# Kernel tuning notes

Measured on AMD Instinct MI355X. Metric: run time of the kernel, lower is better.

The kernel has to match this reference:

```python
import jax, jax.numpy as jnp
import numpy as np

B, S, D, H = 8, 1024, 512, 8
DK = D // H
NEG = -1e30  # stands in for -inf; masked probs are zero-filled afterwards, so math matches


def setup_inputs() -> dict:
    rng = jax.random.key(0)
    ks = jax.random.split(rng, 12)
    f = lambda k, shape: jax.random.normal(k, shape, dtype=jnp.float32)
    w = lambda k: f(k, (D, D)) * 0.02  # stored as (in, out); y = x @ W + b
    return {
        "query": f(ks[0], (B, S, D)),
        "key": f(ks[1], (B, S, D)),
        "value": f(ks[2], (B, S, D)),
        "mask": jax.random.randint(ks[3], (B, 1, S), 0, 2, dtype=jnp.int32),
        "Wq": w(ks[4]), "bq": jnp.zeros((D,), jnp.float32),
        "Wk": w(ks[5]), "bk": jnp.zeros((D,), jnp.float32),
        "Wv": w(ks[6]), "bv": jnp.zeros((D,), jnp.float32),
        "Wo": w(ks[7]), "bo": jnp.zeros((D,), jnp.float32),
    }


def reference(query, key, value, mask, Wq, bq, Wk, bk, Wv, bv, Wo, bo):
    # QKV projections -> (B, H, S, DK)
    def proj(x, W, b):
        return (x @ W + b).reshape(B, -1, H, DK).transpose(0, 2, 1, 3)

    q = proj(query, Wq, bq)
    k = proj(key, Wk, bk)
    v = proj(value, Wv, bv)

    scores = jnp.einsum("bhqd,bhkd->bhqk", q, k) / jnp.sqrt(jnp.float32(DK))
    m = (mask[:, None, :, :] == 0)  # (B, 1, 1, S): True where masked out
    scores = jnp.where(m, NEG, scores)
    attn = jax.nn.softmax(scores, axis=-1)
    attn = jnp.where(m, 0.0, attn)  # dropout rate is 0.0 -> identity

    x = jnp.einsum("bhqk,bhkd->bhqd", attn, v)
    x = x.transpose(0, 2, 1, 3).reshape(B, -1, D)  # (B, S, D)
    return x @ Wo + bo
```

## Files before the change

### kernel.cpp

```cpp
#include <hip/hip_runtime.h>
#include <hip/hip_bf16.h>

#define NB 8
#define NS 1024
#define ND 512
#define NH 8
#define NDK 64

typedef __attribute__((ext_vector_type(8))) short bf16x8;
typedef __attribute__((ext_vector_type(4))) float f32x4;
typedef __attribute__((ext_vector_type(16))) float f32x16;

#define QSCALE 0.18033688011112042f
#define NEGBIG -3.0e38f

#define CVTPK(dst, a, b) \
    asm("v_cvt_pk_bf16_f32 %0, %1, %2" : "=v"(dst) : "v"(a), "v"(b))
#define PLSWAP(a, b) \
    asm("v_permlane32_swap_b32 %0, %1" : "+v"(a), "+v"(b))

__device__ __forceinline__ unsigned short bfround(float f) {
    union { float f; unsigned u; } v; v.f = f;
    unsigned u = v.u;
    u += 0x7fffu + ((u >> 16) & 1u);
    return (unsigned short)(u >> 16);
}


__global__ __launch_bounds__(256) void wt_kernel(const float* __restrict__ W0,
                                                 const float* __restrict__ W1,
                                                 const float* __restrict__ W2,
                                                 const float* __restrict__ W3,
                                                 unsigned short* __restrict__ wt) {
    __shared__ float sh[64][65];
    const int z = blockIdx.z;
    const float* W = z == 0 ? W0 : z == 1 ? W1 : z == 2 ? W2 : W3;
    unsigned short* out = wt + (size_t)z * ND * ND;
    const int o0 = blockIdx.x * 64, i0 = blockIdx.y * 64;
    const int tx = threadIdx.x & 63;
    const int ty = threadIdx.x >> 6;
    #pragma unroll
    for (int rr = 0; rr < 16; ++rr) {
        const int row = ty * 16 + rr;
        sh[row][tx] = W[(size_t)(i0 + row) * ND + o0 + tx];
    }
    __syncthreads();
    #pragma unroll
    for (int rr = 0; rr < 16; ++rr) {
        const int row = ty * 16 + rr;
        out[(size_t)(o0 + row) * ND + i0 + tx] = bfround(sh[tx][row]);
    }
}

__global__ __launch_bounds__(256) void gemm_qkv(
    const float* __restrict__ A0, const float* __restrict__ A1, const float* __restrict__ A2,
    const unsigned short* __restrict__ wt,
    const float* __restrict__ b0, const float* __restrict__ b1, const float* __restrict__ b2,
    unsigned short* __restrict__ outb) {
    __shared__ unsigned short SM[27648];
    const int t = threadIdx.x;
    const int lane = t & 63, w = t >> 6;
    const int wr = w >> 1, wc = w & 1;
    const int lr = lane & 15, lg = lane >> 4;
    const int bid = blockIdx.x;
    const int u = (bid & 7) * 32 + (bid >> 3);
    const int xt = u & 3, yt = u >> 2;
    const int z = blockIdx.y;
    const float* A = z == 0 ? A0 : z == 1 ? A1 : A2;
    const float* bias = z == 0 ? b0 : z == 1 ? b1 : b2;
    const unsigned short* Wt = wt + (size_t)z * ND * ND;
    unsigned short* outp = outb + (size_t)z * NB * NH * NS * NDK;
    const int m0 = yt * 128, n0 = xt * 128;

    const int a_row = t >> 4;
    const int a_col = (t & 15) * 4;
    const int b_row = t >> 3;
    const int b_col = (t & 7) * 8;

    f32x4 acc[4][4];
    #pragma unroll
    for (int i = 0; i < 4; ++i)
        #pragma unroll
        for (int j = 0; j < 4; ++j) acc[i][j] = (f32x4){0.f, 0.f, 0.f, 0.f};

    f32x4 ra[8];
    bf16x8 rbv[4];

#define AL(p) (SM + (p) * 9216)
#define BLS (SM + 18432)

#define QKV_LOAD(kt) do {                                                      \
        const int _k0 = (kt) * 64;                                             \
        _Pragma("unroll")                                                      \
        for (int j = 0; j < 8; ++j)                                            \
            ra[j] = *(const f32x4*)(A + (size_t)(m0 + a_row + j * 16) * ND + _k0 + a_col); \
        _Pragma("unroll")                                                      \
        for (int j = 0; j < 4; ++j)                                            \
            rbv[j] = *(const bf16x8*)(Wt + (size_t)(n0 + b_row + j * 32) * ND + _k0 + b_col); \
    } while (0)

#define QKV_WRITEA(p) do {                                                     \
        _Pragma("unroll")                                                      \
        for (int j = 0; j < 8; ++j) {                                          \
            unsigned c0, c1;                                                   \
            CVTPK(c0, ra[j][0], ra[j][1]);                                     \
            CVTPK(c1, ra[j][2], ra[j][3]);                                     \
            uint2 pv; pv.x = c0; pv.y = c1;                                    \
            *(uint2*)(&AL(p)[(a_row + j * 16) * 72 + a_col]) = pv;             \
        }                                                                      \
    } while (0)

#define QKV_WRITEB() do {                                                      \
        _Pragma("unroll")                                                      \
        for (int j = 0; j < 4; ++j)                                            \
            *(bf16x8*)(&BLS[(b_row + j * 32) * 72 + b_col]) = rbv[j];          \
    } while (0)

#define QKV_COMPUTE(p) do {                                                    \
        _Pragma("unroll")                                                      \
        for (int kk = 0; kk < 2; ++kk) {                                       \
            bf16x8 af[4], bfr[4];                                              \
            _Pragma("unroll")                                                  \
            for (int mi = 0; mi < 4; ++mi)                                     \
                af[mi] = *(const bf16x8*)(&AL(p)[(wr * 64 + mi * 16 + lr) * 72 + kk * 32 + lg * 8]); \
            _Pragma("unroll")                                                  \
            for (int nj = 0; nj < 4; ++nj)                                     \
                bfr[nj] = *(const bf16x8*)(&BLS[(wc * 64 + nj * 16 + lr) * 72 + kk * 32 + lg * 8]); \
            __builtin_amdgcn_s_setprio(1);                                     \
            _Pragma("unroll")                                                  \
            for (int mi = 0; mi < 4; ++mi)                                     \
                _Pragma("unroll")                                              \
                for (int nj = 0; nj < 4; ++nj)                                 \
                    acc[mi][nj] = __builtin_amdgcn_mfma_f32_16x16x32_bf16(     \
                        af[mi], bfr[nj], acc[mi][nj], 0, 0, 0);                \
            __builtin_amdgcn_s_setprio(0);                                     \
        }                                                                      \
    } while (0)

    QKV_LOAD(0);
    QKV_WRITEA(0);
    QKV_WRITEB();
    QKV_LOAD(1);
    __builtin_amdgcn_sched_barrier(0);
    __syncthreads();
    #pragma unroll 1
    for (int kt = 0; kt < 7; ++kt) {
        QKV_COMPUTE(kt & 1);
        __syncthreads();
        QKV_WRITEA((kt + 1) & 1);
        QKV_WRITEB();
        QKV_LOAD(kt + 2 > 7 ? 7 : kt + 2);
        __builtin_amdgcn_sched_barrier(0);
        __syncthreads();
    }
    QKV_COMPUTE(1);
#undef QKV_LOAD
#undef QKV_WRITEA
#undef QKV_WRITEB
#undef QKV_COMPUTE
#undef AL
#undef BLS

    __syncthreads();
    const float osc = z == 0 ? QSCALE : 1.0f;
    const int bb = m0 >> 10;
    const unsigned msb = (unsigned)(m0 & 1023);
    char* const C = (char*)SM;
    if (z <= 1) {
        #pragma unroll
        for (int mi = 0; mi < 4; ++mi)
            #pragma unroll
            for (int nj = 0; nj < 4; ++nj) {
                const int coln = wc * 64 + nj * 16 + lr;
                const float bv = bias[n0 + coln];
                #pragma unroll
                for (int r = 0; r < 4; ++r) {
                    const int row = wr * 64 + mi * 16 + lg * 4 + r;
                    unsigned off = (unsigned)(row * 256 + coln * 2);
                    off ^= (row & 7) << 4;
                    *(unsigned short*)(C + off) = bfround((acc[mi][nj][r] + bv) * osc);
                }
            }
        __syncthreads();
        #pragma unroll
        for (int cc = 0; cc < 8; ++cc) {
            const int c = w * 8 + cc;
            const int sg = c >> 3, hhl = (c >> 2) & 1, kk = c & 3;
            const int row = sg * 32 + (lane & 31);
            unsigned off = (unsigned)(row * 256 + (hhl * 64 + kk * 16 + (lane >> 5) * 8) * 2);
            off ^= (row & 7) << 4;
            const bf16x8 v8 = *(const bf16x8*)(C + off);
            const int hh = xt * 2 + hhl;
            const unsigned chunk = z == 0 ? ((msb >> 5) + sg) * 4 + kk
                                          : ((msb >> 6) + (sg >> 1)) * 8 + (sg & 1) * 4 + kk;
            *(bf16x8*)(outp + (((size_t)(bb * NH + hh)) << 16) +
                       (size_t)chunk * 512 + lane * 8) = v8;
        }
    } else {
        #pragma unroll
        for (int mi = 0; mi < 4; ++mi)
            #pragma unroll
            for (int nj = 0; nj < 4; ++nj) {
                const int dkl = wc * 64 + nj * 16 + lr;
                const float bv = bias[n0 + dkl];
                #pragma unroll
                for (int r = 0; r < 4; ++r) {
                    const int sl = wr * 64 + mi * 16 + lg * 4 + r;
                    unsigned off = (unsigned)(dkl * 256 + sl * 2);
                    off ^= (dkl & 7) << 4;
                    *(unsigned short*)(C + off) = bfround(acc[mi][nj][r] + bv);
                }
            }
        __syncthreads();
        #pragma unroll
        for (int cc = 0; cc < 8; ++cc) {
            const int c = w * 8 + cc;
            const int hhl = c >> 4, s6 = (c >> 3) & 1, od = (c >> 2) & 1, s4 = c & 3;
            const int row = hhl * 64 + od * 32 + (lane & 31);
            unsigned off = (unsigned)(row * 256 + (s6 * 64 + s4 * 16 + (lane >> 5) * 8) * 2);
            off ^= (row & 7) << 4;
            const bf16x8 v8 = *(const bf16x8*)(C + off);
            const int hh = xt * 2 + hhl;
            const unsigned chunk = ((msb >> 6) + s6) * 8 + od * 4 + s4;
            *(bf16x8*)(outp + (((size_t)(bb * NH + hh)) << 16) +
                       (size_t)chunk * 512 + lane * 8) = v8;
        }
    }
}

__global__ __launch_bounds__(256) void gemm_out(
    const unsigned short* __restrict__ Xb, const unsigned short* __restrict__ Wt,
    const float* __restrict__ bo, float* __restrict__ outp) {
    __shared__ unsigned short SM2[10240];
    const int t = threadIdx.x;
    const int lane = t & 63, w = t >> 6;
    const int wr = w >> 1, wc = w & 1;
    const int lr = lane & 15, lg = lane >> 4;
    const int bid = blockIdx.x;
    const int u = (bid & 7) * 128 + (bid >> 3);
    const int xt = u & 7, yt = u >> 3;
    const int m0 = yt * 64, n0 = xt * 64;

    const int s_row = t >> 2;
    const int s_col = (t & 3) * 8;

    f32x4 acc[2][2];
    #pragma unroll
    for (int i = 0; i < 2; ++i)
        #pragma unroll
        for (int j = 0; j < 2; ++j) acc[i][j] = (f32x4){0.f, 0.f, 0.f, 0.f};

    bf16x8 raa, rbb;

#define OUT_LOAD(kt) do {                                                      \
        const int _k0 = (kt) * 32;                                             \
        raa = *(const bf16x8*)(Xb + (size_t)(m0 + s_row) * ND + _k0 + s_col);  \
        rbb = *(const bf16x8*)(Wt + (size_t)(n0 + s_row) * ND + _k0 + s_col);  \
    } while (0)

#define OUT_WRITE(p) do {                                                      \
        *(bf16x8*)(&SM2[(p) * 2560 + s_row * 40 + s_col]) = raa;               \
        *(bf16x8*)(&SM2[5120 + (p) * 2560 + s_row * 40 + s_col]) = rbb;        \
    } while (0)

#define OUT_COMPUTE(p) do {                                                    \
        bf16x8 af[2], bfr[2];                                                  \
        _Pragma("unroll")                                                      \
        for (int mi = 0; mi < 2; ++mi)                                         \
            af[mi] = *(const bf16x8*)(&SM2[(p) * 2560 + (wr * 32 + mi * 16 + lr) * 40 + lg * 8]); \
        _Pragma("unroll")                                                      \
        for (int nj = 0; nj < 2; ++nj)                                         \
            bfr[nj] = *(const bf16x8*)(&SM2[5120 + (p) * 2560 + (wc * 32 + nj * 16 + lr) * 40 + lg * 8]); \
        __builtin_amdgcn_s_setprio(1);                                         \
        _Pragma("unroll")                                                      \
        for (int mi = 0; mi < 2; ++mi)                                         \
            _Pragma("unroll")                                                  \
            for (int nj = 0; nj < 2; ++nj)                                     \
                acc[mi][nj] = __builtin_amdgcn_mfma_f32_16x16x32_bf16(         \
                    af[mi], bfr[nj], acc[mi][nj], 0, 0, 0);                    \
        __builtin_amdgcn_s_setprio(0);                                         \
    } while (0)

    OUT_LOAD(0);
    OUT_WRITE(0);
    OUT_LOAD(1);
    __syncthreads();
    #pragma unroll 1
    for (int kt = 0; kt < 15; ++kt) {
        OUT_COMPUTE(kt & 1);
        OUT_WRITE((kt + 1) & 1);
        if (kt < 14) OUT_LOAD(kt + 2);
        __syncthreads();
    }
    OUT_COMPUTE(1);
#undef OUT_LOAD
#undef OUT_WRITE
#undef OUT_COMPUTE

    #pragma unroll
    for (int mi = 0; mi < 2; ++mi) {
        #pragma unroll
        for (int nj = 0; nj < 2; ++nj) {
            const int n = n0 + wc * 32 + nj * 16 + lr;
            const float bv = bo[n];
            #pragma unroll
            for (int r = 0; r < 4; ++r) {
                const int m = m0 + wr * 32 + mi * 16 + lg * 4 + r;
                outp[(size_t)m * ND + n] = acc[mi][nj][r] + bv;
            }
        }
    }
}

struct AttnState {
    f32x16 acc0, acc1;
    float m_st, l_st;
};

__device__ __forceinline__ void attn_step(const bf16x8 (&kf)[8], const bf16x8 (&vv)[8],
                                          const bf16x8 (&qf)[4], int mval,
                                          float* __restrict__ brow, int lane, int hi,
                                          AttnState& st) {
    brow[lane] = mval ? 0.f : NEGBIG;

    f32x16 sc0 = {}, sc1 = {};
    __builtin_amdgcn_s_setprio(1);
    sc0 = __builtin_amdgcn_mfma_f32_32x32x16_bf16(kf[0], qf[0], sc0, 0, 0, 0);
    sc1 = __builtin_amdgcn_mfma_f32_32x32x16_bf16(kf[4], qf[0], sc1, 0, 0, 0);
    sc0 = __builtin_amdgcn_mfma_f32_32x32x16_bf16(kf[1], qf[1], sc0, 0, 0, 0);
    sc1 = __builtin_amdgcn_mfma_f32_32x32x16_bf16(kf[5], qf[1], sc1, 0, 0, 0);
    sc0 = __builtin_amdgcn_mfma_f32_32x32x16_bf16(kf[2], qf[2], sc0, 0, 0, 0);
    sc1 = __builtin_amdgcn_mfma_f32_32x32x16_bf16(kf[6], qf[2], sc1, 0, 0, 0);
    sc0 = __builtin_amdgcn_mfma_f32_32x32x16_bf16(kf[3], qf[3], sc0, 0, 0, 0);
    sc1 = __builtin_amdgcn_mfma_f32_32x32x16_bf16(kf[7], qf[3], sc1, 0, 0, 0);
    __builtin_amdgcn_s_setprio(0);

    {
        const float* bl = brow + 4 * hi;
        #pragma unroll
        for (int mm = 0; mm < 4; ++mm) {
            const f32x4 bv0 = *(const f32x4*)(bl + 8 * mm);
            const f32x4 bv1 = *(const f32x4*)(bl + 32 + 8 * mm);
            #pragma unroll
            for (int c = 0; c < 4; ++c) {
                sc0[4 * mm + c] += bv0[c];
                sc1[4 * mm + c] += bv1[c];
            }
        }
    }

    float tv[16];
    #pragma unroll
    for (int r = 0; r < 16; ++r) tv[r] = fmaxf(sc0[r], sc1[r]);
    #pragma unroll
    for (int s = 8; s > 0; s >>= 1)
        #pragma unroll
        for (int r = 0; r < 16; ++r)
            if (r < s) tv[r] = fmaxf(tv[r], tv[r + s]);
    const float mx = fmaxf(tv[0], __shfl_xor(tv[0], 32));
    const float mn = fmaxf(st.m_st, mx);

    #pragma unroll
    for (int r = 0; r < 16; ++r) {
        sc0[r] = __builtin_amdgcn_exp2f(sc0[r] - mn);
        sc1[r] = __builtin_amdgcn_exp2f(sc1[r] - mn);
    }
    #pragma unroll
    for (int r = 0; r < 16; ++r) tv[r] = sc0[r] + sc1[r];
    #pragma unroll
    for (int s = 8; s > 0; s >>= 1)
        #pragma unroll
        for (int r = 0; r < 16; ++r)
            if (r < s) tv[r] += tv[r + s];
    const float rs = tv[0] + __shfl_xor(tv[0], 32);

    const bool ch = mn > st.m_st;
    if (__any(ch)) {
        const float f = __builtin_amdgcn_exp2f(st.m_st - mn);
        st.l_st = st.l_st * f + rs;
        st.m_st = mn;
        #pragma unroll
        for (int r = 0; r < 16; ++r) { st.acc0[r] *= f; st.acc1[r] *= f; }
    } else {
        st.l_st += rs;
    }

    union U8 { unsigned u[4]; bf16x8 v; };
    bf16x8 pA0, pA1, pB0, pB1;
    {
        unsigned w00, w01, w10, w11, w20, w21, w30, w31;
        CVTPK(w00, sc0[0], sc0[1]);  CVTPK(w01, sc0[2], sc0[3]);
        CVTPK(w10, sc0[4], sc0[5]);  CVTPK(w11, sc0[6], sc0[7]);
        CVTPK(w20, sc0[8], sc0[9]);  CVTPK(w21, sc0[10], sc0[11]);
        CVTPK(w30, sc0[12], sc0[13]); CVTPK(w31, sc0[14], sc0[15]);
        PLSWAP(w00, w10); PLSWAP(w01, w11);
        PLSWAP(w20, w30); PLSWAP(w21, w31);
        U8 f0; f0.u[0] = w00; f0.u[1] = w01; f0.u[2] = w10; f0.u[3] = w11;
        U8 f1; f1.u[0] = w20; f1.u[1] = w21; f1.u[2] = w30; f1.u[3] = w31;
        pA0 = f0.v; pA1 = f1.v;
    }
    {
        unsigned w00, w01, w10, w11, w20, w21, w30, w31;
        CVTPK(w00, sc1[0], sc1[1]);  CVTPK(w01, sc1[2], sc1[3]);
        CVTPK(w10, sc1[4], sc1[5]);  CVTPK(w11, sc1[6], sc1[7]);
        CVTPK(w20, sc1[8], sc1[9]);  CVTPK(w21, sc1[10], sc1[11]);
        CVTPK(w30, sc1[12], sc1[13]); CVTPK(w31, sc1[14], sc1[15]);
        PLSWAP(w00, w10); PLSWAP(w01, w11);
        PLSWAP(w20, w30); PLSWAP(w21, w31);
        U8 f0; f0.u[0] = w00; f0.u[1] = w01; f0.u[2] = w10; f0.u[3] = w11;
        U8 f1; f1.u[0] = w20; f1.u[1] = w21; f1.u[2] = w30; f1.u[3] = w31;
        pB0 = f0.v; pB1 = f1.v;
    }

    __builtin_amdgcn_s_setprio(1);
    st.acc0 = __builtin_amdgcn_mfma_f32_32x32x16_bf16(vv[0], pA0, st.acc0, 0, 0, 0);
    st.acc1 = __builtin_amdgcn_mfma_f32_32x32x16_bf16(vv[4], pA0, st.acc1, 0, 0, 0);
    st.acc0 = __builtin_amdgcn_mfma_f32_32x32x16_bf16(vv[1], pA1, st.acc0, 0, 0, 0);
    st.acc1 = __builtin_amdgcn_mfma_f32_32x32x16_bf16(vv[5], pA1, st.acc1, 0, 0, 0);
    st.acc0 = __builtin_amdgcn_mfma_f32_32x32x16_bf16(vv[2], pB0, st.acc0, 0, 0, 0);
    st.acc1 = __builtin_amdgcn_mfma_f32_32x32x16_bf16(vv[6], pB0, st.acc1, 0, 0, 0);
    st.acc0 = __builtin_amdgcn_mfma_f32_32x32x16_bf16(vv[3], pB1, st.acc0, 0, 0, 0);
    st.acc1 = __builtin_amdgcn_mfma_f32_32x32x16_bf16(vv[7], pB1, st.acc1, 0, 0, 0);
    __builtin_amdgcn_s_setprio(0);
}

__global__ __launch_bounds__(256, 2) void attn_kernel(const unsigned short* __restrict__ QF,
                                                      const unsigned short* __restrict__ KF,
                                                      const unsigned short* __restrict__ VF,
                                                      const int* __restrict__ mask,
                                                      unsigned short* __restrict__ Xb) {
    __shared__ float bias_lds[4][64];
    const int t = threadIdx.x;
    const int lane = t & 63, w = t >> 6;
    const int q32 = lane & 31, hi = lane >> 5;
    const int bid = blockIdx.x;
    const int u = (bid & 7) * 64 + (bid >> 3);
    const int bh = u >> 3, xq = u & 7;
    const int b = bh >> 3, h = bh & 7;
    const int q = xq * 128 + w * 32 + q32;
    const unsigned short* QFh = QF + ((size_t)bh << 16);
    const unsigned short* KFh = KF + ((size_t)bh << 16);
    const unsigned short* VFh = VF + ((size_t)bh << 16);
    const int* mk = mask + b * NS;
    float* brow = &bias_lds[w][0];

    bf16x8 qf[4];
    {
        const unsigned short* Qp = QFh + (size_t)(xq * 16 + w * 4) * 512 + lane * 8;
        qf[0] = *(const bf16x8*)(Qp + 0 * 512);
        qf[1] = *(const bf16x8*)(Qp + 1 * 512);
        qf[2] = *(const bf16x8*)(Qp + 2 * 512);
        qf[3] = *(const bf16x8*)(Qp + 3 * 512);
    }

    AttnState st;
    st.acc0 = (f32x16){}; st.acc1 = (f32x16){};
    st.m_st = -1.0e30f; st.l_st = 0.f;

    bf16x8 kA[8], kB[8], vv[8];

#define LOADK(dst, itx) do {                                                   \
        const unsigned short* _p = KFh + (size_t)(itx) * 4096 + lane * 8;      \
        dst[0] = *(const bf16x8*)(_p + 0 * 512);                               \
        dst[1] = *(const bf16x8*)(_p + 1 * 512);                               \
        dst[2] = *(const bf16x8*)(_p + 2 * 512);                               \
        dst[3] = *(const bf16x8*)(_p + 3 * 512);                               \
        dst[4] = *(const bf16x8*)(_p + 4 * 512);                               \
        dst[5] = *(const bf16x8*)(_p + 5 * 512);                               \
        dst[6] = *(const bf16x8*)(_p + 6 * 512);                               \
        dst[7] = *(const bf16x8*)(_p + 7 * 512);                               \
    } while (0)

#define LOADV(dst, itx) do {                                                   \
        const unsigned short* _p = VFh + (size_t)(itx) * 4096 + lane * 8;      \
        dst[0] = *(const bf16x8*)(_p + 0 * 512);                               \
        dst[1] = *(const bf16x8*)(_p + 1 * 512);                               \
        dst[2] = *(const bf16x8*)(_p + 2 * 512);                               \
        dst[3] = *(const bf16x8*)(_p + 3 * 512);                               \
        dst[4] = *(const bf16x8*)(_p + 4 * 512);                               \
        dst[5] = *(const bf16x8*)(_p + 5 * 512);                               \
        dst[6] = *(const bf16x8*)(_p + 6 * 512);                               \
        dst[7] = *(const bf16x8*)(_p + 7 * 512);                               \
    } while (0)

    LOADK(kA, 0);
    #pragma unroll 1
    for (int ii = 0; ii < 8; ++ii) {
        const int itE = ii * 2, itO = itE + 1;
        const int mE = mk[itE * 64 + lane];
        LOADV(vv, itE);
        LOADK(kB, itO);
        __builtin_amdgcn_sched_barrier(0);
        attn_step(kA, vv, qf, mE, brow, lane, hi, st);
        const int mO = mk[itO * 64 + lane];
        const int itN = itO + 1 > 15 ? 15 : itO + 1;
        LOADV(vv, itO);
        LOADK(kA, itN);
        __builtin_amdgcn_sched_barrier(0);
        attn_step(kB, vv, qf, mO, brow, lane, hi, st);
    }
#undef LOADK
#undef LOADV

    const float inv = st.l_st > 0.f ? 1.f / st.l_st : 0.f;
    unsigned short* Xp = Xb + (size_t)(b * NS + q) * ND + h * 64 + 4 * hi;
    #pragma unroll
    for (int mm = 0; mm < 4; ++mm) {
        unsigned w0, w1;
        CVTPK(w0, st.acc0[4 * mm] * inv, st.acc0[4 * mm + 1] * inv);
        CVTPK(w1, st.acc0[4 * mm + 2] * inv, st.acc0[4 * mm + 3] * inv);
        uint2 pv; pv.x = w0; pv.y = w1;
        *(uint2*)(Xp + 8 * mm) = pv;
        CVTPK(w0, st.acc1[4 * mm] * inv, st.acc1[4 * mm + 1] * inv);
        CVTPK(w1, st.acc1[4 * mm + 2] * inv, st.acc1[4 * mm + 3] * inv);
        pv.x = w0; pv.y = w1;
        *(uint2*)(Xp + 32 + 8 * mm) = pv;
    }
}

extern "C" void kernel_launch(void* const* d_in, const int* in_sizes, int n_in,
                              void* d_out, int out_size, void* d_ws, size_t ws_size,
                              hipStream_t stream) {
    const float* query = (const float*)d_in[0];
    const float* key   = (const float*)d_in[1];
    const float* value = (const float*)d_in[2];
    const int*   mask  = (const int*)d_in[3];
    const float* Wq = (const float*)d_in[4];
    const float* bq = (const float*)d_in[5];
    const float* Wk = (const float*)d_in[6];
    const float* bk = (const float*)d_in[7];
    const float* Wv = (const float*)d_in[8];
    const float* bv = (const float*)d_in[9];
    const float* Wo = (const float*)d_in[10];
    const float* bo = (const float*)d_in[11];

    const size_t HEADSZ = (size_t)NB * NH * NS * NDK;
    unsigned short* wt = (unsigned short*)d_ws;
    unsigned short* QFb = wt + (size_t)4 * ND * ND;
    unsigned short* KFb = QFb + HEADSZ;
    unsigned short* VFb = KFb + HEADSZ;
    unsigned short* Xb  = VFb + HEADSZ;

    wt_kernel<<<dim3(8, 8, 4), 256, 0, stream>>>(Wq, Wk, Wv, Wo, wt);

    gemm_qkv<<<dim3(256, 3), 256, 0, stream>>>(query, key, value, wt, bq, bk, bv, QFb);

    attn_kernel<<<512, 256, 0, stream>>>(QFb, KFb, VFb, mask, Xb);

    gemm_out<<<1024, 256, 0, stream>>>(Xb, wt + (size_t)3 * ND * ND, bo, (float*)d_out);
}
```

Measured before the change: 77.76 us.

## Stage K/V tiles through LDS with async global_load_lds double buffering

The attention kernel stops having each wave load the full K and V tiles from global memory into registers. Instead the four waves of a block cooperatively copy each 64-key K/V tile into a double-buffered LDS area with global_load_lds, wait on vmcnt and a barrier, then read the fragments from LDS. This cuts redundant global/L2 traffic across waves sharing a head. The mask bias for all keys is now precomputed once into LDS, and launch bounds rise to allow three blocks per CU. In exchange it adds two block barriers per iteration and more LDS use per block, which may limit overlap and occupancy.

```diff
diff --git a/kernel.cpp b/kernel.cpp
--- a/kernel.cpp
+++ b/kernel.cpp
@@ -18,6 +18,15 @@
     asm("v_cvt_pk_bf16_f32 %0, %1, %2" : "=v"(dst) : "v"(a), "v"(b))
 #define PLSWAP(a, b) \
     asm("v_permlane32_swap_b32 %0, %1" : "+v"(a), "+v"(b))
+#define GLOAD16(gp, lp)                                                        \
+    __builtin_amdgcn_global_load_lds(                                          \
+        (const __attribute__((address_space(1))) unsigned*)(gp),               \
+        (__attribute__((address_space(3))) unsigned*)(lp), 16, 0, 0)
+#define VMCNT0() asm volatile("s_waitcnt vmcnt(0)" ::: "memory")
+#define VMCNT4() asm volatile("s_waitcnt vmcnt(4)" ::: "memory")
+#define LGKM0()  asm volatile("s_waitcnt lgkmcnt(0)" ::: "memory")
+#define SBAR() __builtin_amdgcn_s_barrier()
+#define SCHED0() __builtin_amdgcn_sched_barrier(0)
 
 __device__ __forceinline__ unsigned short bfround(float f) {
     union { float f; unsigned u; } v; v.f = f;
@@ -182,6 +191,8 @@
                 }
             }
         __syncthreads();
+        const unsigned cb = 0;
+        (void)cb;
         #pragma unroll
         for (int cc = 0; cc < 8; ++cc) {
             const int c = w * 8 + cc;
@@ -312,124 +323,13 @@
     }
 }
 
-struct AttnState {
-    f32x16 acc0, acc1;
-    float m_st, l_st;
-};
-
-__device__ __forceinline__ void attn_step(const bf16x8 (&kf)[8], const bf16x8 (&vv)[8],
-                                          const bf16x8 (&qf)[4], int mval,
-                                          float* __restrict__ brow, int lane, int hi,
-                                          AttnState& st) {
-    brow[lane] = mval ? 0.f : NEGBIG;
-
-    f32x16 sc0 = {}, sc1 = {};
-    __builtin_amdgcn_s_setprio(1);
-    sc0 = __builtin_amdgcn_mfma_f32_32x32x16_bf16(kf[0], qf[0], sc0, 0, 0, 0);
-    sc1 = __builtin_amdgcn_mfma_f32_32x32x16_bf16(kf[4], qf[0], sc1, 0, 0, 0);
-    sc0 = __builtin_amdgcn_mfma_f32_32x32x16_bf16(kf[1], qf[1], sc0, 0, 0, 0);
-    sc1 = __builtin_amdgcn_mfma_f32_32x32x16_bf16(kf[5], qf[1], sc1, 0, 0, 0);
-    sc0 = __builtin_amdgcn_mfma_f32_32x32x16_bf16(kf[2], qf[2], sc0, 0, 0, 0);
-    sc1 = __builtin_amdgcn_mfma_f32_32x32x16_bf16(kf[6], qf[2], sc1, 0, 0, 0);
-    sc0 = __builtin_amdgcn_mfma_f32_32x32x16_bf16(kf[3], qf[3], sc0, 0, 0, 0);
-    sc1 = __builtin_amdgcn_mfma_f32_32x32x16_bf16(kf[7], qf[3], sc1, 0, 0, 0);
-    __builtin_amdgcn_s_setprio(0);
-
-    {
-        const float* bl = brow + 4 * hi;
-        #pragma unroll
-        for (int mm = 0; mm < 4; ++mm) {
-            const f32x4 bv0 = *(const f32x4*)(bl + 8 * mm);
-            const f32x4 bv1 = *(const f32x4*)(bl + 32 + 8 * mm);
-            #pragma unroll
-            for (int c = 0; c < 4; ++c) {
-                sc0[4 * mm + c] += bv0[c];
-                sc1[4 * mm + c] += bv1[c];
-            }
-        }
-    }
-
-    float tv[16];
-    #pragma unroll
-    for (int r = 0; r < 16; ++r) tv[r] = fmaxf(sc0[r], sc1[r]);
-    #pragma unroll
-    for (int s = 8; s > 0; s >>= 1)
-        #pragma unroll
-        for (int r = 0; r < 16; ++r)
-            if (r < s) tv[r] = fmaxf(tv[r], tv[r + s]);
-    const float mx = fmaxf(tv[0], __shfl_xor(tv[0], 32));
-    const float mn = fmaxf(st.m_st, mx);
-
-    #pragma unroll
-    for (int r = 0; r < 16; ++r) {
-        sc0[r] = __builtin_amdgcn_exp2f(sc0[r] - mn);
-        sc1[r] = __builtin_amdgcn_exp2f(sc1[r] - mn);
-    }
-    #pragma unroll
-    for (int r = 0; r < 16; ++r) tv[r] = sc0[r] + sc1[r];
-    #pragma unroll
-    for (int s = 8; s > 0; s >>= 1)
-        #pragma unroll
-        for (int r = 0; r < 16; ++r)
-            if (r < s) tv[r] += tv[r + s];
-    const float rs = tv[0] + __shfl_xor(tv[0], 32);
-
-    const bool ch = mn > st.m_st;
-    if (__any(ch)) {
-        const float f = __builtin_amdgcn_exp2f(st.m_st - mn);
-        st.l_st = st.l_st * f + rs;
-        st.m_st = mn;
-        #pragma unroll
-        for (int r = 0; r < 16; ++r) { st.acc0[r] *= f; st.acc1[r] *= f; }
-    } else {
-        st.l_st += rs;
-    }
-
-    union U8 { unsigned u[4]; bf16x8 v; };
-    bf16x8 pA0, pA1, pB0, pB1;
-    {
-        unsigned w00, w01, w10, w11, w20, w21, w30, w31;
-        CVTPK(w00, sc0[0], sc0[1]);  CVTPK(w01, sc0[2], sc0[3]);
-        CVTPK(w10, sc0[4], sc0[5]);  CVTPK(w11, sc0[6], sc0[7]);
-        CVTPK(w20, sc0[8], sc0[9]);  CVTPK(w21, sc0[10], sc0[11]);
-        CVTPK(w30, sc0[12], sc0[13]); CVTPK(w31, sc0[14], sc0[15]);
-        PLSWAP(w00, w10); PLSWAP(w01, w11);
-        PLSWAP(w20, w30); PLSWAP(w21, w31);
-        U8 f0; f0.u[0] = w00; f0.u[1] = w01; f0.u[2] = w10; f0.u[3] = w11;
-        U8 f1; f1.u[0] = w20; f1.u[1] = w21; f1.u[2] = w30; f1.u[3] = w31;
-        pA0 = f0.v; pA1 = f1.v;
-    }
-    {
-        unsigned w00, w01, w10, w11, w20, w21, w30, w31;
-        CVTPK(w00, sc1[0], sc1[1]);  CVTPK(w01, sc1[2], sc1[3]);
-        CVTPK(w10, sc1[4], sc1[5]);  CVTPK(w11, sc1[6], sc1[7]);
-        CVTPK(w20, sc1[8], sc1[9]);  CVTPK(w21, sc1[10], sc1[11]);
-        CVTPK(w30, sc1[12], sc1[13]); CVTPK(w31, sc1[14], sc1[15]);
-        PLSWAP(w00, w10); PLSWAP(w01, w11);
-        PLSWAP(w20, w30); PLSWAP(w21, w31);
-        U8 f0; f0.u[0] = w00; f0.u[1] = w01; f0.u[2] = w10; f0.u[3] = w11;
-        U8 f1; f1.u[0] = w20; f1.u[1] = w21; f1.u[2] = w30; f1.u[3] = w31;
-        pB0 = f0.v; pB1 = f1.v;
-    }
-
-    __builtin_amdgcn_s_setprio(1);
-    st.acc0 = __builtin_amdgcn_mfma_f32_32x32x16_bf16(vv[0], pA0, st.acc0, 0, 0, 0);
-    st.acc1 = __builtin_amdgcn_mfma_f32_32x32x16_bf16(vv[4], pA0, st.acc1, 0, 0, 0);
-    st.acc0 = __builtin_amdgcn_mfma_f32_32x32x16_bf16(vv[1], pA1, st.acc0, 0, 0, 0);
-    st.acc1 = __builtin_amdgcn_mfma_f32_32x32x16_bf16(vv[5], pA1, st.acc1, 0, 0, 0);
-    st.acc0 = __builtin_amdgcn_mfma_f32_32x32x16_bf16(vv[2], pB0, st.acc0, 0, 0, 0);
-    st.acc1 = __builtin_amdgcn_mfma_f32_32x32x16_bf16(vv[6], pB0, st.acc1, 0, 0, 0);
-    st.acc0 = __builtin_amdgcn_mfma_f32_32x32x16_bf16(vv[3], pB1, st.acc0, 0, 0, 0);
-    st.acc1 = __builtin_amdgcn_mfma_f32_32x32x16_bf16(vv[7], pB1, st.acc1, 0, 0, 0);
-    __builtin_amdgcn_s_setprio(0);
-}
-
-__global__ __launch_bounds__(256, 2) void attn_kernel(const unsigned short* __restrict__ QF,
+__global__ __launch_bounds__(256, 3) void attn_kernel(const unsigned short* __restrict__ QF,
                                                       const unsigned short* __restrict__ KF,
                                                       const unsigned short* __restrict__ VF,
                                                       const int* __restrict__ mask,
                                                       unsigned short* __restrict__ Xb) {
-    __shared__ float bias_lds[4][64];
+    __shared__ unsigned short KV[16384];
+    __shared__ float biasl[1024];
     const int t = threadIdx.x;
     const int lane = t & 63, w = t >> 6;
     const int q32 = lane & 31, hi = lane >> 5;
@@ -442,7 +342,12 @@
     const unsigned short* KFh = KF + ((size_t)bh << 16);
     const unsigned short* VFh = VF + ((size_t)bh << 16);
     const int* mk = mask + b * NS;
-    float* brow = &bias_lds[w][0];
+
+    #pragma unroll
+    for (int i = 0; i < 4; ++i) {
+        const int idx = t + i * 256;
+        biasl[idx] = mk[idx] ? 0.f : NEGBIG;
+    }
 
     bf16x8 qf[4];
     {
@@ -453,66 +358,155 @@
         qf[3] = *(const bf16x8*)(Qp + 3 * 512);
     }
 
-    AttnState st;
-    st.acc0 = (f32x16){}; st.acc1 = (f32x16){};
-    st.m_st = -1.0e30f; st.l_st = 0.f;
-
-    bf16x8 kA[8], kB[8], vv[8];
-
-#define LOADK(dst, itx) do {                                                   \
-        const unsigned short* _p = KFh + (size_t)(itx) * 4096 + lane * 8;      \
-        dst[0] = *(const bf16x8*)(_p + 0 * 512);                               \
-        dst[1] = *(const bf16x8*)(_p + 1 * 512);                               \
-        dst[2] = *(const bf16x8*)(_p + 2 * 512);                               \
-        dst[3] = *(const bf16x8*)(_p + 3 * 512);                               \
-        dst[4] = *(const bf16x8*)(_p + 4 * 512);                               \
-        dst[5] = *(const bf16x8*)(_p + 5 * 512);                               \
-        dst[6] = *(const bf16x8*)(_p + 6 * 512);                               \
-        dst[7] = *(const bf16x8*)(_p + 7 * 512);                               \
-    } while (0)
-
-#define LOADV(dst, itx) do {                                                   \
-        const unsigned short* _p = VFh + (size_t)(itx) * 4096 + lane * 8;      \
-        dst[0] = *(const bf16x8*)(_p + 0 * 512);                               \
-        dst[1] = *(const bf16x8*)(_p + 1 * 512);                               \
-        dst[2] = *(const bf16x8*)(_p + 2 * 512);                               \
-        dst[3] = *(const bf16x8*)(_p + 3 * 512);                               \
-        dst[4] = *(const bf16x8*)(_p + 4 * 512);                               \
-        dst[5] = *(const bf16x8*)(_p + 5 * 512);                               \
-        dst[6] = *(const bf16x8*)(_p + 6 * 512);                               \
-        dst[7] = *(const bf16x8*)(_p + 7 * 512);                               \
-    } while (0)
-
-    LOADK(kA, 0);
+    f32x16 acc0 = {}, acc1 = {};
+    float m_st = -1.0e30f, l_st = 0.f;
+
+#define STAGE(p, itx) do {                                                     \
+        const unsigned short* _ks = KFh + (size_t)(itx) * 4096 + (w * 2) * 512 + lane * 8; \
+        GLOAD16(_ks, &KV[(p) * 4096 + (w * 2) * 512]);                         \
+        GLOAD16(_ks + 512, &KV[(p) * 4096 + (w * 2 + 1) * 512]);               \
+        const unsigned short* _vs = VFh + (size_t)(itx) * 4096 + (w * 2) * 512 + lane * 8; \
+        GLOAD16(_vs, &KV[8192 + (p) * 4096 + (w * 2) * 512]);                  \
+        GLOAD16(_vs + 512, &KV[8192 + (p) * 4096 + (w * 2 + 1) * 512]);        \
+    } while (0)
+
+    STAGE(0, 0);
+    LGKM0();
     #pragma unroll 1
-    for (int ii = 0; ii < 8; ++ii) {
-        const int itE = ii * 2, itO = itE + 1;
-        const int mE = mk[itE * 64 + lane];
-        LOADV(vv, itE);
-        LOADK(kB, itO);
-        __builtin_amdgcn_sched_barrier(0);
-        attn_step(kA, vv, qf, mE, brow, lane, hi, st);
-        const int mO = mk[itO * 64 + lane];
-        const int itN = itO + 1 > 15 ? 15 : itO + 1;
-        LOADV(vv, itO);
-        LOADK(kA, itN);
-        __builtin_amdgcn_sched_barrier(0);
-        attn_step(kB, vv, qf, mO, brow, lane, hi, st);
-    }
-#undef LOADK
-#undef LOADV
-
-    const float inv = st.l_st > 0.f ? 1.f / st.l_st : 0.f;
+    for (int it = 0; it < 16; ++it) {
+        const int p = it & 1;
+        if (it < 15) {
+            STAGE(p ^ 1, it + 1);
+            SCHED0();
+            VMCNT4();
+        } else {
+            VMCNT0();
+        }
+        SBAR();
+
+        bf16x8 kf[8];
+        #pragma unroll
+        for (int j = 0; j < 8; ++j)
+            kf[j] = *(const bf16x8*)(&KV[p * 4096 + j * 512 + lane * 8]);
+        f32x16 sc0 = {}, sc1 = {};
+        __builtin_amdgcn_s_setprio(1);
+        sc0 = __builtin_amdgcn_mfma_f32_32x32x16_bf16(kf[0], qf[0], sc0, 0, 0, 0);
+        sc1 = __builtin_amdgcn_mfma_f32_32x32x16_bf16(kf[4], qf[0], sc1, 0, 0, 0);
+        sc0 = __builtin_amdgcn_mfma_f32_32x32x16_bf16(kf[1], qf[1], sc0, 0, 0, 0);
+        sc1 = __builtin_amdgcn_mfma_f32_32x32x16_bf16(kf[5], qf[1], sc1, 0, 0, 0);
+        sc0 = __builtin_amdgcn_mfma_f32_32x32x16_bf16(kf[2], qf[2], sc0, 0, 0, 0);
+        sc1 = __builtin_amdgcn_mfma_f32_32x32x16_bf16(kf[6], qf[2], sc1, 0, 0, 0);
+        sc0 = __builtin_amdgcn_mfma_f32_32x32x16_bf16(kf[3], qf[3], sc0, 0, 0, 0);
+        sc1 = __builtin_amdgcn_mfma_f32_32x32x16_bf16(kf[7], qf[3], sc1, 0, 0, 0);
+        __builtin_amdgcn_s_setprio(0);
+
+        {
+            const float* bl = &biasl[it * 64 + 4 * hi];
+            #pragma unroll
+            for (int mm = 0; mm < 4; ++mm) {
+                const f32x4 bv0 = *(const f32x4*)(bl + 8 * mm);
+                const f32x4 bv1 = *(const f32x4*)(bl + 32 + 8 * mm);
+                #pragma unroll
+                for (int c = 0; c < 4; ++c) {
+                    sc0[4 * mm + c] += bv0[c];
+                    sc1[4 * mm + c] += bv1[c];
+                }
+            }
+        }
+
+        float tv[16];
+        #pragma unroll
+        for (int r = 0; r < 16; ++r) tv[r] = fmaxf(sc0[r], sc1[r]);
+        #pragma unroll
+        for (int s = 8; s > 0; s >>= 1)
+            #pragma unroll
+            for (int r = 0; r < 16; ++r)
+                if (r < s) tv[r] = fmaxf(tv[r], tv[r + s]);
+        const float mx = fmaxf(tv[0], __shfl_xor(tv[0], 32));
+        const float mn = fmaxf(m_st, mx);
+
+        #pragma unroll
+        for (int r = 0; r < 16; ++r) {
+            sc0[r] = __builtin_amdgcn_exp2f(sc0[r] - mn);
+            sc1[r] = __builtin_amdgcn_exp2f(sc1[r] - mn);
+        }
+        #pragma unroll
+        for (int r = 0; r < 16; ++r) tv[r] = sc0[r] + sc1[r];
+        #pragma unroll
+        for (int s = 8; s > 0; s >>= 1)
+            #pragma unroll
+            for (int r = 0; r < 16; ++r)
+                if (r < s) tv[r] += tv[r + s];
+        const float rs = tv[0] + __shfl_xor(tv[0], 32);
+
+        const bool ch = mn > m_st;
+        if (__any(ch)) {
+            const float f = __builtin_amdgcn_exp2f(m_st - mn);
+            l_st = l_st * f + rs;
+            m_st = mn;
+            #pragma unroll
+            for (int r = 0; r < 16; ++r) { acc0[r] *= f; acc1[r] *= f; }
+        } else {
+            l_st += rs;
+        }
+
+        union U8 { unsigned u[4]; bf16x8 v; };
+        bf16x8 pA0, pA1, pB0, pB1;
+        {
+            unsigned w00, w01, w10, w11, w20, w21, w30, w31;
+            CVTPK(w00, sc0[0], sc0[1]);  CVTPK(w01, sc0[2], sc0[3]);
+            CVTPK(w10, sc0[4], sc0[5]);  CVTPK(w11, sc0[6], sc0[7]);
+            CVTPK(w20, sc0[8], sc0[9]);  CVTPK(w21, sc0[10], sc0[11]);
+            CVTPK(w30, sc0[12], sc0[13]); CVTPK(w31, sc0[14], sc0[15]);
+            PLSWAP(w00, w10); PLSWAP(w01, w11);
+            PLSWAP(w20, w30); PLSWAP(w21, w31);
+            U8 f0; f0.u[0] = w00; f0.u[1] = w01; f0.u[2] = w10; f0.u[3] = w11;
+            U8 f1; f1.u[0] = w20; f1.u[1] = w21; f1.u[2] = w30; f1.u[3] = w31;
+            pA0 = f0.v; pA1 = f1.v;
+        }
+        {
+            unsigned w00, w01, w10, w11, w20, w21, w30, w31;
+            CVTPK(w00, sc1[0], sc1[1]);  CVTPK(w01, sc1[2], sc1[3]);
+            CVTPK(w10, sc1[4], sc1[5]);  CVTPK(w11, sc1[6], sc1[7]);
+            CVTPK(w20, sc1[8], sc1[9]);  CVTPK(w21, sc1[10], sc1[11]);
+            CVTPK(w30, sc1[12], sc1[13]); CVTPK(w31, sc1[14], sc1[15]);
+            PLSWAP(w00, w10); PLSWAP(w01, w11);
+            PLSWAP(w20, w30); PLSWAP(w21, w31);
+            U8 f0; f0.u[0] = w00; f0.u[1] = w01; f0.u[2] = w10; f0.u[3] = w11;
+            U8 f1; f1.u[0] = w20; f1.u[1] = w21; f1.u[2] = w30; f1.u[3] = w31;
+            pB0 = f0.v; pB1 = f1.v;
+        }
+
+        bf16x8 vf[8];
+        #pragma unroll
+        for (int j = 0; j < 8; ++j)
+            vf[j] = *(const bf16x8*)(&KV[8192 + p * 4096 + j * 512 + lane * 8]);
+        __builtin_amdgcn_s_setprio(1);
+        acc0 = __builtin_amdgcn_mfma_f32_32x32x16_bf16(vf[0], pA0, acc0, 0, 0, 0);
+        acc1 = __builtin_amdgcn_mfma_f32_32x32x16_bf16(vf[4], pA0, acc1, 0, 0, 0);
+        acc0 = __builtin_amdgcn_mfma_f32_32x32x16_bf16(vf[1], pA1, acc0, 0, 0, 0);
+        acc1 = __builtin_amdgcn_mfma_f32_32x32x16_bf16(vf[5], pA1, acc1, 0, 0, 0);
+        acc0 = __builtin_amdgcn_mfma_f32_32x32x16_bf16(vf[2], pB0, acc0, 0, 0, 0);
+        acc1 = __builtin_amdgcn_mfma_f32_32x32x16_bf16(vf[6], pB0, acc1, 0, 0, 0);
+        acc0 = __builtin_amdgcn_mfma_f32_32x32x16_bf16(vf[3], pB1, acc0, 0, 0, 0);
+        acc1 = __builtin_amdgcn_mfma_f32_32x32x16_bf16(vf[7], pB1, acc1, 0, 0, 0);
+        __builtin_amdgcn_s_setprio(0);
+
+        SBAR();
+    }
+#undef STAGE
+
+    const float inv = l_st > 0.f ? 1.f / l_st : 0.f;
     unsigned short* Xp = Xb + (size_t)(b * NS + q) * ND + h * 64 + 4 * hi;
     #pragma unroll
     for (int mm = 0; mm < 4; ++mm) {
         unsigned w0, w1;
-        CVTPK(w0, st.acc0[4 * mm] * inv, st.acc0[4 * mm + 1] * inv);
-        CVTPK(w1, st.acc0[4 * mm + 2] * inv, st.acc0[4 * mm + 3] * inv);
+        CVTPK(w0, acc0[4 * mm] * inv, acc0[4 * mm + 1] * inv);
+        CVTPK(w1, acc0[4 * mm + 2] * inv, acc0[4 * mm + 3] * inv);
         uint2 pv; pv.x = w0; pv.y = w1;
         *(uint2*)(Xp + 8 * mm) = pv;
-        CVTPK(w0, st.acc1[4 * mm] * inv, st.acc1[4 * mm + 1] * inv);
-        CVTPK(w1, st.acc1[4 * mm + 2] * inv, st.acc1[4 * mm + 3] * inv);
+        CVTPK(w0, acc1[4 * mm] * inv, acc1[4 * mm + 1] * inv);
+        CVTPK(w1, acc1[4 * mm + 2] * inv, acc1[4 * mm + 3] * inv);
         pv.x = w0; pv.y = w1;
         *(uint2*)(Xp + 32 + 8 * mm) = pv;
     }
```

New measurement: 79.92 us. +2.8%, slower.
